# Kernel optimization log

Hardware: AMD Instinct MI355X
Metric: run time of the kernel (lower is better)

The kernel has to match this reference:

```python
import jax, jax.numpy as jnp
import numpy as np

B, N, D = 8, 65536, 3
K = 64                 # num_centers
NPOINT = 4096
M = NPOINT // K * 2    # max_neighbors = 128
S = NPOINT // K        # fps samples per group = 64
NITER = 10             # KMeans default Niter


def _sqdist(src, dst):
    # ||s||^2 + ||d||^2 - 2 s.d   (same math as (s-d)^2 sum, GEMM form)
    s2 = (src ** 2).sum(-1)[:, :, None]          # [B,N,1]
    d2 = (dst ** 2).sum(-1)[:, None, :]          # [B,1,K]
    return s2 + d2 - 2.0 * jnp.einsum('bnd,bkd->bnk', src, dst)


def _kmeans(x):
    Bb, Nn, Dd = x.shape
    c = x[:, :K, :]
    bidx = jnp.arange(Bb)[:, None]               # broadcast with cl [B,N]
    for _ in range(NITER):
        cl = jnp.argmin(_sqdist(x, c), axis=2)   # [B,N] cluster codes
        c = jnp.zeros((Bb, K, Dd), x.dtype).at[bidx, cl].add(x)
        ncl = jnp.zeros((Bb, K), x.dtype).at[bidx, cl].add(1.0)
        c = c / ncl[:, :, None]
    return c


def _query_neighbor(x, centers):
    dist = _sqdist(x, centers)                   # [B,N,K]
    negd = -jnp.transpose(dist, (0, 2, 1))       # [B,K,N]
    _, nidx = jax.lax.top_k(negd, M)             # M nearest points per center
    bidx = jnp.arange(x.shape[0])[:, None, None]
    return x[bidx, nidx]                         # [B,K,M,3]


def _batch_fps(xyz, farthest0):
    # xyz: [B,G,Nn,3]; sequential farthest-point sampling per group
    Bb, G, Nn, _ = xyz.shape
    dist0 = jnp.full((Bb, G, Nn), 1e10, xyz.dtype)

    def step(carry, _):
        distance, farthest = carry
        centroid = jnp.take_along_axis(xyz, farthest[:, :, None, None], axis=2)  # [B,G,1,3]
        d = ((xyz - centroid) ** 2).sum(-1)       # [B,G,Nn]
        distance = jnp.minimum(distance, d)
        new_far = jnp.argmax(distance, -1).astype(farthest.dtype)
        return (distance, new_far), farthest      # store index BEFORE update

    _, idx = jax.lax.scan(step, (dist0, farthest0), None, length=S)
    idx = jnp.transpose(idx, (1, 2, 0))           # [B,G,S]
    idx3 = jnp.broadcast_to(idx[..., None], idx.shape + (3,))
    new_xyz = jnp.take_along_axis(xyz, idx3, axis=2)  # [B,G,S,3]
    return new_xyz.reshape(Bb, G * S, 3)


def setup_inputs() -> dict:
    key = jax.random.key(0)
    k1, k2 = jax.random.split(key)
    x = jax.random.normal(k1, (B, N, D), dtype=jnp.float32)
    farthest0 = jax.random.randint(k2, (B, K), 0, M, dtype=jnp.int32)
    return {"x": x, "farthest0": farthest0}


def reference(x, farthest0):
    centers = _kmeans(x)                  # [B,K,3]
    neighbor = _query_neighbor(x, centers)  # [B,K,M,3]
    new_xyz = _batch_fps(neighbor, farthest0)  # [B, NPOINT, 3]
    return new_xyz, centers
```

## Files before the change

### kernel.cpp

```cpp
#include <hip/hip_runtime.h>
#include <stdint.h>

#pragma clang fp contract(off)

#define B 8
#define N 65536
#define KC 64
#define M 128
#define S 64
#define NITER 10
#define TOPK_T 1024
#define NWAVES (TOPK_T / 64)
#define HPAD 257
#define CAP 2048
#define UPD_T 1024
#define RANGE 16384
#define NRANGE (N / RANGE)
#define PPT (RANGE / UPD_T)
#define GBATCH 2048

using u32 = unsigned int;
using u64 = unsigned long long;

__device__ __forceinline__ float sq3(float a, float b, float c) {
  return __fadd_rn(__fadd_rn(__fmul_rn(a, a), __fmul_rn(b, b)), __fmul_rn(c, c));
}
__device__ __forceinline__ float dot3(float x0, float x1, float x2,
                                      float c0, float c1, float c2) {
  return __fadd_rn(__fadd_rn(__fmul_rn(x0, c0), __fmul_rn(x1, c1)), __fmul_rn(x2, c2));
}
__device__ __forceinline__ float distf(float s2, float d2, float dt) {
  return __fsub_rn(__fadd_rn(s2, d2), __fmul_rn(2.0f, dt));
}
__device__ __forceinline__ u32 fkey(float f) {
  u32 u = __float_as_uint(f);
  return (u & 0x80000000u) ? ~u : (u | 0x80000000u);
}


__global__ void k_init_centers(const float* __restrict__ x, float* __restrict__ centers) {
  int i = blockIdx.x * blockDim.x + threadIdx.x;
  if (i >= B * KC * 3) return;
  int b = i / (KC * 3);
  int r = i % (KC * 3);
  centers[i] = x[(size_t)b * N * 3 + r];
}

__global__ void k_s2(const float* __restrict__ x, float* __restrict__ s2) {
  int i = blockIdx.x * blockDim.x + threadIdx.x;
  const float2* x2 = (const float2*)x;
  float2 A = x2[3 * i], Bv = x2[3 * i + 1], C = x2[3 * i + 2];
  float2 o;
  o.x = sq3(A.x, A.y, Bv.x);
  o.y = sq3(Bv.y, C.x, C.y);
  ((float2*)s2)[i] = o;
}

__global__ void k_assign(const float* __restrict__ x, const float* __restrict__ centers,
                         unsigned char* __restrict__ cl) {
  __shared__ float4 cs[KC];
  int b = blockIdx.x >> 7;
  int chunk = blockIdx.x & 127;
  int t = threadIdx.x;
  if (t < KC) {
    float a0 = centers[(b * KC + t) * 3 + 0];
    float a1 = centers[(b * KC + t) * 3 + 1];
    float a2 = centers[(b * KC + t) * 3 + 2];
    cs[t] = make_float4(a0, a1, a2, sq3(a0, a1, a2));
  }
  __syncthreads();
  int pr = chunk * 256 + t;
  const float2* xb2 = (const float2*)(x + (size_t)b * N * 3);
  float2 A = xb2[3 * pr], Bv = xb2[3 * pr + 1], C = xb2[3 * pr + 2];
  float s20 = sq3(A.x, A.y, Bv.x);
  float s21 = sq3(Bv.y, C.x, C.y);
  float best0 = __int_as_float(0x7f800000), best1 = best0;
  int bi0 = 0, bi1 = 0;
  for (int k = 0; k < KC; ++k) {
    float4 cc = cs[k];
    float d0 = distf(s20, cc.w, dot3(A.x, A.y, Bv.x, cc.x, cc.y, cc.z));
    float d1 = distf(s21, cc.w, dot3(Bv.y, C.x, C.y, cc.x, cc.y, cc.z));
    if (d0 < best0) { best0 = d0; bi0 = k; }
    if (d1 < best1) { best1 = d1; bi1 = k; }
  }
  *(unsigned short*)(cl + (size_t)b * N + 2 * pr) =
      (unsigned short)(bi0 | (bi1 << 8));
}

__global__ __launch_bounds__(UPD_T)
void k_cluster_update(const float* __restrict__ x, const unsigned char* __restrict__ cl,
                      float* __restrict__ centers) {
  __shared__ unsigned short midx[RANGE];
  __shared__ float bcoord[3][GBATCH + 1];
  __shared__ int woff[NWAVES];
  __shared__ int sCnt;
  int g = blockIdx.x;
  int bk = ((g & 7) << 6) | (g >> 3);
  int b = bk >> 6, k = bk & 63;
  int t = threadIdx.x, lane = t & 63, wid = t >> 6;
  const unsigned char* clb = cl + (size_t)b * N;
  const float* xb = x + (size_t)b * N * 3;
  float acc = 0.f;
  int cntAll = 0;

  for (int r = 0; r < NRANGE; ++r) {
    const uint4* cp = (const uint4*)(clb + r * RANGE);
    uint4 v = cp[t];
    u32 wsv[4] = {v.x, v.y, v.z, v.w};
    int m = 0;
#pragma unroll
    for (int j = 0; j < PPT; ++j)
      m += (((wsv[j >> 2] >> ((j & 3) * 8)) & 255u) == (u32)k);
    int incl = m;
#pragma unroll
    for (int o = 1; o < 64; o <<= 1) {
      int u = __shfl_up(incl, o);
      if (lane >= o) incl += u;
    }
    if (lane == 63) woff[wid] = incl;
    __syncthreads();
    if (t == 0) {
      int run = 0;
      for (int w = 0; w < NWAVES; ++w) { int vv = woff[w]; woff[w] = run; run += vv; }
      sCnt = run;
    }
    __syncthreads();
    int off = woff[wid] + incl - m;
    int mcnt = sCnt;
    int base = t * PPT;
#pragma unroll
    for (int j = 0; j < PPT; ++j) {
      if (((wsv[j >> 2] >> ((j & 3) * 8)) & 255u) == (u32)k)
        midx[off++] = (unsigned short)(base + j);
    }
    __syncthreads();
    for (int bo = 0; bo < mcnt; bo += GBATCH) {
      int bn = min(GBATCH, mcnt - bo);
      for (int i = t; i < bn; i += UPD_T) {
        int li = midx[bo + i];
        size_t src = ((size_t)(r * RANGE + li)) * 3;
        bcoord[0][i] = xb[src];
        bcoord[1][i] = xb[src + 1];
        bcoord[2][i] = xb[src + 2];
      }
      __syncthreads();
      if (wid == 0 && lane < 3) {
        const float* mb = &bcoord[lane][0];
        for (int i = 0; i < bn; ++i) acc = __fadd_rn(acc, mb[i]);
      }
      __syncthreads();
    }
    cntAll += mcnt;
    __syncthreads();
  }
  if (wid == 0 && lane < 3)
    centers[bk * 3 + lane] = __fdiv_rn(acc, (float)cntAll);
}

__global__ __launch_bounds__(TOPK_T)
void k_query_topk(const float* __restrict__ x, const float* __restrict__ s2g,
                  const float* __restrict__ centers, float* __restrict__ neighbor) {
  __shared__ u32 whist[NWAVES * HPAD];
  __shared__ u32 hist[256];
  __shared__ u64 lessList[M];
  __shared__ u64 candList[CAP];
  __shared__ u32 eqList[256];
  __shared__ u32 sPrefix;
  __shared__ int sNeed, sCntBin;
  __shared__ int cntLess, cntEq;
  __shared__ float sc0, sc1, sc2, sd2;

  int g = blockIdx.x;
  int bk = ((g & 7) << 6) | (g >> 3);
  int b = bk >> 6;
  int t = threadIdx.x;
  int lane = t & 63, wid = t >> 6;
  if (t == 0) {
    float c0 = centers[bk * 3], c1 = centers[bk * 3 + 1], c2 = centers[bk * 3 + 2];
    sc0 = c0; sc1 = c1; sc2 = c2; sd2 = sq3(c0, c1, c2);
    cntLess = 0; cntEq = 0;
  }
  for (int i = t; i < NWAVES * HPAD; i += TOPK_T) whist[i] = 0;
  __syncthreads();
  float c0 = sc0, c1 = sc1, c2 = sc2, d2 = sd2;
  const float* xb = x + (size_t)b * N * 3;
  const float2* xb2 = (const float2*)xb;
  const float2* s2b2 = (const float2*)(s2g + (size_t)b * N);

  for (int p = t; p < N / 2; p += TOPK_T) {
    float2 A = xb2[3 * p], Bv = xb2[3 * p + 1], C = xb2[3 * p + 2];
    float2 s2p = s2b2[p];
    float d0 = distf(s2p.x, d2, dot3(A.x, A.y, Bv.x, c0, c1, c2));
    float d1 = distf(s2p.y, d2, dot3(Bv.y, C.x, C.y, c0, c1, c2));
    u32 b0 = fkey(d0) >> 24;
    u32 b1 = fkey(d1) >> 24;
    u64 lt = ((u64)1 << lane) - 1;
    u64 eq0 = ~0ull, eq1 = ~0ull;
#pragma unroll
    for (int i = 0; i < 8; ++i) {
      u64 m0 = __ballot((b0 >> i) & 1);
      u64 m1 = __ballot((b1 >> i) & 1);
      eq0 &= ((b0 >> i) & 1) ? m0 : ~m0;
      eq1 &= ((b1 >> i) & 1) ? m1 : ~m1;
    }
    if ((eq0 & lt) == 0) whist[wid * HPAD + b0] += (u32)__popcll(eq0);
    if ((eq1 & lt) == 0) whist[wid * HPAD + b1] += (u32)__popcll(eq1);
  }
  __syncthreads();
  if (t < 256) {
    u32 s = 0;
#pragma unroll
    for (int w = 0; w < NWAVES; ++w) s += whist[w * HPAD + t];
    hist[t] = s;
  }
  __syncthreads();
  if (t == 0) {
    int cum = 0;
    for (int bin = 0; bin < 256; ++bin) {
      int c = (int)hist[bin];
      if (cum + c >= M) { sPrefix = (u32)bin; sNeed = M - cum; sCntBin = c; break; }
      cum += c;
    }
  }
  __syncthreads();
  u32 selByte = sPrefix;
  int needEq = sNeed;
  int cntBin = sCntBin;

  if (cntBin <= CAP) {
    for (int p = t; p < N / 2; p += TOPK_T) {
      float2 A = xb2[3 * p], Bv = xb2[3 * p + 1], C = xb2[3 * p + 2];
      float2 s2p = s2b2[p];
      float d0 = distf(s2p.x, d2, dot3(A.x, A.y, Bv.x, c0, c1, c2));
      float d1 = distf(s2p.y, d2, dot3(Bv.y, C.x, C.y, c0, c1, c2));
      u32 key0 = fkey(d0), key1 = fkey(d1);
      u32 pb0 = key0 >> 24, pb1 = key1 >> 24;
      if (pb0 < selByte) {
        int q = atomicAdd(&cntLess, 1);
        lessList[q] = ((u64)key0 << 32) | (u32)(2 * p);
      } else if (pb0 == selByte) {
        int q = atomicAdd(&cntEq, 1);
        candList[q] = ((u64)key0 << 32) | (u32)(2 * p);
      }
      if (pb1 < selByte) {
        int q = atomicAdd(&cntLess, 1);
        lessList[q] = ((u64)key1 << 32) | (u32)(2 * p + 1);
      } else if (pb1 == selByte) {
        int q = atomicAdd(&cntEq, 1);
        candList[q] = ((u64)key1 << 32) | (u32)(2 * p + 1);
      }
    }
    __syncthreads();
    int nl = cntLess;
    int ne = cntEq;
    int P = 1; while (P < ne) P <<= 1;
    for (int i = t; i < M; i += TOPK_T) if (i >= nl) lessList[i] = ~0ull;
    for (int i = t; i < P; i += TOPK_T) if (i >= ne) candList[i] = ~0ull;
    __syncthreads();
    for (int ksz = 2; ksz <= M; ksz <<= 1) {
      for (int j = ksz >> 1; j > 0; j >>= 1) {
        for (int idx = t; idx < M; idx += TOPK_T) {
          int ixj = idx ^ j;
          if (ixj > idx) {
            u64 a = lessList[idx], bb = lessList[ixj];
            bool up = ((idx & ksz) == 0);
            if (up ? (a > bb) : (a < bb)) { lessList[idx] = bb; lessList[ixj] = a; }
          }
        }
        __syncthreads();
      }
    }
    for (int ksz = 2; ksz <= P; ksz <<= 1) {
      for (int j = ksz >> 1; j > 0; j >>= 1) {
        for (int idx = t; idx < P; idx += TOPK_T) {
          int ixj = idx ^ j;
          if (ixj > idx) {
            u64 a = candList[idx], bb = candList[ixj];
            bool up = ((idx & ksz) == 0);
            if (up ? (a > bb) : (a < bb)) { candList[idx] = bb; candList[ixj] = a; }
          }
        }
        __syncthreads();
      }
    }
    if (t < M) {
      u64 e = (t < nl) ? lessList[t] : candList[t - nl];
      int idx = (int)(e & 0xFFFFFFFFu);
      size_t src = ((size_t)b * N + idx) * 3;
      size_t dst = ((size_t)bk * M + t) * 3;
      neighbor[dst]     = x[src];
      neighbor[dst + 1] = x[src + 1];
      neighbor[dst + 2] = x[src + 2];
    }
    return;
  }

  u32 prefix = selByte << 24;
  int need = needEq;
  for (int r = 2; r >= 0; --r) {
    for (int i = t; i < 256; i += TOPK_T) hist[i] = 0;
    __syncthreads();
    int sh = r * 8;
    for (int n = t; n < N; n += TOPK_T) {
      float x0 = xb[n * 3], x1 = xb[n * 3 + 1], x2 = xb[n * 3 + 2];
      float d = distf(sq3(x0, x1, x2), d2, dot3(x0, x1, x2, c0, c1, c2));
      u32 key = fkey(d);
      if ((key >> (sh + 8)) == (prefix >> (sh + 8)))
        atomicAdd(&hist[(key >> sh) & 255u], 1u);
    }
    __syncthreads();
    if (t == 0) {
      int cum = 0;
      for (int bin = 0; bin < 256; ++bin) {
        int c = (int)hist[bin];
        if (cum + c >= need) { sPrefix = prefix | ((u32)bin << sh); sNeed = need - cum; break; }
        cum += c;
      }
    }
    __syncthreads();
    prefix = sPrefix; need = sNeed;
    __syncthreads();
  }
  u32 K128 = prefix;

  if (t == 0) { cntLess = 0; cntEq = 0; }
  __syncthreads();
  for (int n = t; n < N; n += TOPK_T) {
    float x0 = xb[n * 3], x1 = xb[n * 3 + 1], x2 = xb[n * 3 + 2];
    float d = distf(sq3(x0, x1, x2), d2, dot3(x0, x1, x2, c0, c1, c2));
    u32 key = fkey(d);
    if (key < K128) {
      int p = atomicAdd(&cntLess, 1);
      if (p < M) lessList[p] = ((u64)key << 32) | (u32)n;
    } else if (key == K128) {
      int p = atomicAdd(&cntEq, 1);
      if (p < 256) eqList[p] = (u32)n;
    }
  }
  __syncthreads();
  int nl = cntLess;
  int ne = cntEq;
  for (int i = t; i < M; i += TOPK_T) if (i >= nl) lessList[i] = ~0ull;
  for (int i = t; i < 256; i += TOPK_T) if (i >= ne) eqList[i] = 0xFFFFFFFFu;
  __syncthreads();

  for (int ksz = 2; ksz <= M; ksz <<= 1) {
    for (int j = ksz >> 1; j > 0; j >>= 1) {
      for (int idx = t; idx < M; idx += TOPK_T) {
        int ixj = idx ^ j;
        if (ixj > idx) {
          u64 a = lessList[idx], bb = lessList[ixj];
          bool up = ((idx & ksz) == 0);
          if (up ? (a > bb) : (a < bb)) { lessList[idx] = bb; lessList[ixj] = a; }
        }
      }
      __syncthreads();
    }
  }
  for (int ksz = 2; ksz <= 256; ksz <<= 1) {
    for (int j = ksz >> 1; j > 0; j >>= 1) {
      for (int idx = t; idx < 256; idx += TOPK_T) {
        int ixj = idx ^ j;
        if (ixj > idx) {
          u32 a = eqList[idx], bb = eqList[ixj];
          bool up = ((idx & ksz) == 0);
          if (up ? (a > bb) : (a < bb)) { eqList[idx] = bb; eqList[ixj] = a; }
        }
      }
      __syncthreads();
    }
  }

  if (t < M) {
    int idx = (t < nl) ? (int)(lessList[t] & 0xFFFFFFFFu) : (int)eqList[t - nl];
    size_t src = ((size_t)b * N + idx) * 3;
    size_t dst = ((size_t)bk * M + t) * 3;
    neighbor[dst]     = x[src];
    neighbor[dst + 1] = x[src + 1];
    neighbor[dst + 2] = x[src + 2];
  }
}

__global__ void k_fps(const float* __restrict__ neighbor, const int* __restrict__ farthest0,
                      const float* __restrict__ centers, float* __restrict__ out) {
  __shared__ float px[M], py[M], pz[M];
  __shared__ float wv[2];
  __shared__ int wi[2];
  int bg = blockIdx.x;
  int b = bg >> 6, g = bg & 63;
  int t = threadIdx.x;
  {
    int i = bg * 128 + t;
    if (i < B * KC * 3) out[B * 4096 * 3 + i] = centers[i];
  }
  size_t src = ((size_t)bg * M + t) * 3;
  float mx = neighbor[src], my = neighbor[src + 1], mz = neighbor[src + 2];
  px[t] = mx; py[t] = my; pz[t] = mz;
  int far = farthest0[bg];
  float dist = 1e10f;
  __syncthreads();
  for (int s = 0; s < S; ++s) {
    if (t == far) {
      size_t dst = ((size_t)b * 4096 + g * 64 + s) * 3;
      out[dst] = mx; out[dst + 1] = my; out[dst + 2] = mz;
    }
    float cx = px[far], cy = py[far], cz = pz[far];
    float dx = __fsub_rn(mx, cx), dy = __fsub_rn(my, cy), dz = __fsub_rn(mz, cz);
    float d = sq3(dx, dy, dz);
    dist = fminf(dist, d);
    float v = dist;
    int i = t;
#pragma unroll
    for (int off = 1; off < 64; off <<= 1) {
      float ov = __shfl_xor(v, off);
      int oi = __shfl_xor(i, off);
      if (ov > v || (ov == v && oi < i)) { v = ov; i = oi; }
    }
    int wid = t >> 6;
    if ((t & 63) == 0) { wv[wid] = v; wi[wid] = i; }
    __syncthreads();
    float v0 = wv[0]; int i0 = wi[0];
    float v1 = wv[1]; int i1 = wi[1];
    far = (v1 > v0 || (v1 == v0 && i1 < i0)) ? i1 : i0;
    __syncthreads();
  }
}

extern "C" void kernel_launch(void* const* d_in, const int* in_sizes, int n_in,
                              void* d_out, int out_size, void* d_ws, size_t ws_size,
                              hipStream_t stream) {
  const float* x = (const float*)d_in[0];
  const int* farthest0 = (const int*)d_in[1];
  float* out = (float*)d_out;

  char* w = (char*)d_ws;
  float* centers         = (float*)(w);
  unsigned char* cl      = (unsigned char*)(w + 8192);
  float* s2              = (float*)(w + 8192 + 524288);
  float* neighbor        = (float*)(w + 8192 + 524288 + 2097152);

  k_init_centers<<<6, 256, 0, stream>>>(x, centers);
  k_s2<<<B * N / 2 / 256, 256, 0, stream>>>(x, s2);
  for (int it = 0; it < NITER; ++it) {
    k_assign<<<B * 128, 256, 0, stream>>>(x, centers, cl);
    k_cluster_update<<<B * KC, UPD_T, 0, stream>>>(x, cl, centers);
  }
  k_query_topk<<<B * KC, TOPK_T, 0, stream>>>(x, s2, centers, neighbor);
  k_fps<<<B * KC, M, 0, stream>>>(neighbor, farthest0, centers, out);
}
```

Before: 560.8 us.

## Estimate top-k threshold from a point sample before a single full candidate pass

The query top-k kernel now builds its radix histogram from only the first 8192 points and refines a 32-bit key threshold on the sampled keys. It then makes one full pass collecting every point at or below that threshold and bitonic-sorts the candidates, falling back to a full four-level radix select when they overflow capacity. This replaces a full-dataset histogram pass plus collection pass with a cheap sample pass plus one full pass. The risk is that a poor sample makes the threshold too loose, too many candidates, or too tight, fewer than 128, which leads to the slower fallback path or to wrong results. The assign kernel's block-to-batch mapping is also interleaved.

Result: no change. 552.4 us (-1.5%).

```diff
diff --git a/kernel.cpp b/kernel.cpp
--- a/kernel.cpp
+++ b/kernel.cpp
@@ -12,6 +12,8 @@
 #define TOPK_T 1024
 #define NWAVES (TOPK_T / 64)
 #define HPAD 257
+#define SAMPLE 8192
+#define SCAP 2048
 #define CAP 2048
 #define UPD_T 1024
 #define RANGE 16384
@@ -59,8 +61,9 @@
 __global__ void k_assign(const float* __restrict__ x, const float* __restrict__ centers,
                          unsigned char* __restrict__ cl) {
   __shared__ float4 cs[KC];
-  int b = blockIdx.x >> 7;
-  int chunk = blockIdx.x & 127;
+  int g = blockIdx.x;
+  int b = g & 7;
+  int chunk = g >> 3;
   int t = threadIdx.x;
   if (t < KC) {
     float a0 = centers[(b * KC + t) * 3 + 0];
@@ -162,23 +165,24 @@
                   const float* __restrict__ centers, float* __restrict__ neighbor) {
   __shared__ u32 whist[NWAVES * HPAD];
   __shared__ u32 hist[256];
+  __shared__ u32 skeys[SCAP];
+  __shared__ u64 candList[CAP];
   __shared__ u64 lessList[M];
-  __shared__ u64 candList[CAP];
   __shared__ u32 eqList[256];
   __shared__ u32 sPrefix;
   __shared__ int sNeed, sCntBin;
-  __shared__ int cntLess, cntEq;
+  __shared__ int cntCand, cntLess, cntEq;
   __shared__ float sc0, sc1, sc2, sd2;
 
   int g = blockIdx.x;
   int bk = ((g & 7) << 6) | (g >> 3);
   int b = bk >> 6;
   int t = threadIdx.x;
-  int lane = t & 63, wid = t >> 6;
+  int wid = t >> 6;
   if (t == 0) {
     float c0 = centers[bk * 3], c1 = centers[bk * 3 + 1], c2 = centers[bk * 3 + 2];
     sc0 = c0; sc1 = c1; sc2 = c2; sd2 = sq3(c0, c1, c2);
-    cntLess = 0; cntEq = 0;
+    cntCand = 0; cntLess = 0; cntEq = 0;
   }
   for (int i = t; i < NWAVES * HPAD; i += TOPK_T) whist[i] = 0;
   __syncthreads();
@@ -187,24 +191,13 @@
   const float2* xb2 = (const float2*)xb;
   const float2* s2b2 = (const float2*)(s2g + (size_t)b * N);
 
-  for (int p = t; p < N / 2; p += TOPK_T) {
+  for (int p = t; p < SAMPLE / 2; p += TOPK_T) {
     float2 A = xb2[3 * p], Bv = xb2[3 * p + 1], C = xb2[3 * p + 2];
     float2 s2p = s2b2[p];
     float d0 = distf(s2p.x, d2, dot3(A.x, A.y, Bv.x, c0, c1, c2));
     float d1 = distf(s2p.y, d2, dot3(Bv.y, C.x, C.y, c0, c1, c2));
-    u32 b0 = fkey(d0) >> 24;
-    u32 b1 = fkey(d1) >> 24;
-    u64 lt = ((u64)1 << lane) - 1;
-    u64 eq0 = ~0ull, eq1 = ~0ull;
-#pragma unroll
-    for (int i = 0; i < 8; ++i) {
-      u64 m0 = __ballot((b0 >> i) & 1);
-      u64 m1 = __ballot((b1 >> i) & 1);
-      eq0 &= ((b0 >> i) & 1) ? m0 : ~m0;
-      eq1 &= ((b1 >> i) & 1) ? m1 : ~m1;
-    }
-    if ((eq0 & lt) == 0) whist[wid * HPAD + b0] += (u32)__popcll(eq0);
-    if ((eq1 & lt) == 0) whist[wid * HPAD + b1] += (u32)__popcll(eq1);
+    atomicAdd(&whist[wid * HPAD + (fkey(d0) >> 24)], 1u);
+    atomicAdd(&whist[wid * HPAD + (fkey(d1) >> 24)], 1u);
   }
   __syncthreads();
   if (t < 256) {
@@ -227,49 +220,70 @@
   int needEq = sNeed;
   int cntBin = sCntBin;
 
-  if (cntBin <= CAP) {
-    for (int p = t; p < N / 2; p += TOPK_T) {
+  u32 thrK;
+  if (cntBin <= SCAP) {
+    for (int p = t; p < SAMPLE / 2; p += TOPK_T) {
       float2 A = xb2[3 * p], Bv = xb2[3 * p + 1], C = xb2[3 * p + 2];
       float2 s2p = s2b2[p];
       float d0 = distf(s2p.x, d2, dot3(A.x, A.y, Bv.x, c0, c1, c2));
       float d1 = distf(s2p.y, d2, dot3(Bv.y, C.x, C.y, c0, c1, c2));
-      u32 key0 = fkey(d0), key1 = fkey(d1);
-      u32 pb0 = key0 >> 24, pb1 = key1 >> 24;
-      if (pb0 < selByte) {
-        int q = atomicAdd(&cntLess, 1);
-        lessList[q] = ((u64)key0 << 32) | (u32)(2 * p);
-      } else if (pb0 == selByte) {
-        int q = atomicAdd(&cntEq, 1);
-        candList[q] = ((u64)key0 << 32) | (u32)(2 * p);
-      }
-      if (pb1 < selByte) {
-        int q = atomicAdd(&cntLess, 1);
-        lessList[q] = ((u64)key1 << 32) | (u32)(2 * p + 1);
-      } else if (pb1 == selByte) {
-        int q = atomicAdd(&cntEq, 1);
-        candList[q] = ((u64)key1 << 32) | (u32)(2 * p + 1);
-      }
-    }
-    __syncthreads();
-    int nl = cntLess;
+      u32 k0 = fkey(d0), k1 = fkey(d1);
+      if ((k0 >> 24) == selByte) skeys[atomicAdd(&cntEq, 1)] = k0;
+      if ((k1 >> 24) == selByte) skeys[atomicAdd(&cntEq, 1)] = k1;
+    }
+    __syncthreads();
     int ne = cntEq;
-    int P = 1; while (P < ne) P <<= 1;
-    for (int i = t; i < M; i += TOPK_T) if (i >= nl) lessList[i] = ~0ull;
-    for (int i = t; i < P; i += TOPK_T) if (i >= ne) candList[i] = ~0ull;
-    __syncthreads();
-    for (int ksz = 2; ksz <= M; ksz <<= 1) {
-      for (int j = ksz >> 1; j > 0; j >>= 1) {
-        for (int idx = t; idx < M; idx += TOPK_T) {
-          int ixj = idx ^ j;
-          if (ixj > idx) {
-            u64 a = lessList[idx], bb = lessList[ixj];
-            bool up = ((idx & ksz) == 0);
-            if (up ? (a > bb) : (a < bb)) { lessList[idx] = bb; lessList[ixj] = a; }
-          }
+    u32 prefix = selByte << 24;
+    int need = needEq;
+    for (int sh = 16; sh >= 0; sh -= 8) {
+      for (int i = t; i < 256; i += TOPK_T) hist[i] = 0;
+      __syncthreads();
+      for (int i = t; i < ne; i += TOPK_T) {
+        u32 kk = skeys[i];
+        if ((kk >> (sh + 8)) == (prefix >> (sh + 8)))
+          atomicAdd(&hist[(kk >> sh) & 255u], 1u);
+      }
+      __syncthreads();
+      if (t == 0) {
+        int cum = 0;
+        for (int bin = 0; bin < 256; ++bin) {
+          int c = (int)hist[bin];
+          if (cum + c >= need) { sPrefix = prefix | ((u32)bin << sh); sNeed = need - cum; break; }
+          cum += c;
         }
-        __syncthreads();
-      }
-    }
+      }
+      __syncthreads();
+      prefix = sPrefix; need = sNeed;
+      __syncthreads();
+    }
+    thrK = prefix;
+  } else {
+    thrK = (selByte << 24) | 0x00FFFFFFu;
+  }
+
+  for (int p = t; p < N / 2; p += TOPK_T) {
+    float2 A = xb2[3 * p], Bv = xb2[3 * p + 1], C = xb2[3 * p + 2];
+    float2 s2p = s2b2[p];
+    float d0 = distf(s2p.x, d2, dot3(A.x, A.y, Bv.x, c0, c1, c2));
+    float d1 = distf(s2p.y, d2, dot3(Bv.y, C.x, C.y, c0, c1, c2));
+    u32 k0 = fkey(d0), k1 = fkey(d1);
+    if (k0 <= thrK) {
+      int q = atomicAdd(&cntCand, 1);
+      if (q < CAP) candList[q] = ((u64)k0 << 32) | (u32)(2 * p);
+    }
+    if (k1 <= thrK) {
+      int q = atomicAdd(&cntCand, 1);
+      if (q < CAP) candList[q] = ((u64)k1 << 32) | (u32)(2 * p + 1);
+    }
+  }
+  __syncthreads();
+  int cc = cntCand;
+
+  if (cc <= CAP) {
+    int P = 1; while (P < cc) P <<= 1;
+    if (P < M) P = M;
+    for (int i = t; i < P; i += TOPK_T) if (i >= cc) candList[i] = ~0ull;
+    __syncthreads();
     for (int ksz = 2; ksz <= P; ksz <<= 1) {
       for (int j = ksz >> 1; j > 0; j >>= 1) {
         for (int idx = t; idx < P; idx += TOPK_T) {
@@ -284,8 +298,7 @@
       }
     }
     if (t < M) {
-      u64 e = (t < nl) ? lessList[t] : candList[t - nl];
-      int idx = (int)(e & 0xFFFFFFFFu);
+      int idx = (int)(candList[t] & 0xFFFFFFFFu);
       size_t src = ((size_t)b * N + idx) * 3;
       size_t dst = ((size_t)bk * M + t) * 3;
       neighbor[dst]     = x[src];
@@ -295,9 +308,9 @@
     return;
   }
 
-  u32 prefix = selByte << 24;
-  int need = needEq;
-  for (int r = 2; r >= 0; --r) {
+  u32 prefix = 0;
+  int need = M;
+  for (int r = 3; r >= 0; --r) {
     for (int i = t; i < 256; i += TOPK_T) hist[i] = 0;
     __syncthreads();
     int sh = r * 8;
@@ -305,8 +318,8 @@
       float x0 = xb[n * 3], x1 = xb[n * 3 + 1], x2 = xb[n * 3 + 2];
       float d = distf(sq3(x0, x1, x2), d2, dot3(x0, x1, x2, c0, c1, c2));
       u32 key = fkey(d);
-      if ((key >> (sh + 8)) == (prefix >> (sh + 8)))
-        atomicAdd(&hist[(key >> sh) & 255u], 1u);
+      bool ok = (r == 3) || ((key >> (sh + 8)) == (prefix >> (sh + 8)));
+      if (ok) atomicAdd(&hist[(key >> sh) & 255u], 1u);
     }
     __syncthreads();
     if (t == 0) {
@@ -339,9 +352,9 @@
   }
   __syncthreads();
   int nl = cntLess;
-  int ne = cntEq;
+  int ne2 = cntEq;
   for (int i = t; i < M; i += TOPK_T) if (i >= nl) lessList[i] = ~0ull;
-  for (int i = t; i < 256; i += TOPK_T) if (i >= ne) eqList[i] = 0xFFFFFFFFu;
+  for (int i = t; i < 256; i += TOPK_T) if (i >= ne2) eqList[i] = 0xFFFFFFFFu;
   __syncthreads();
 
   for (int ksz = 2; ksz <= M; ksz <<= 1) {
```
